# Kernel optimization log

Hardware: AMD Instinct MI355X
Metric: run time of the kernel (lower is better)

Reference implementation:

```python
import jax, jax.numpy as jnp
import numpy as np

B, T, D = 4, 2048, 2048
H = 16
DH = D // H  # 128
THETA = 10000.0


def _rope(x, offset=0):
    # x: [b, h, t, d]; lucidrains rotary_embedding_torch style (interleaved pairs)
    d = x.shape[-1]
    t = x.shape[-2]
    inv_freq = 1.0 / (THETA ** (jnp.arange(0, d, 2, dtype=jnp.float32) / d))  # [d/2]
    pos = jnp.arange(offset, offset + t, dtype=jnp.float32)
    freqs = pos[:, None] * inv_freq[None, :]              # [t, d/2]
    freqs = jnp.repeat(freqs, 2, axis=-1)                 # [t, d] (n r) interleave
    cos = jnp.cos(freqs).astype(x.dtype)
    sin = jnp.sin(freqs).astype(x.dtype)
    x1 = x[..., 0::2]
    x2 = x[..., 1::2]
    rot = jnp.stack([-x2, x1], axis=-1).reshape(x.shape)  # rotate_half
    return x * cos + rot * sin


def setup_inputs() -> dict:
    key = jax.random.key(0)
    ks = jax.random.split(key, 5)
    s = 1.0 / np.sqrt(D)
    return {
        "x": jax.random.normal(ks[0], (B, T, D), jnp.float32),
        "Wq": jax.random.normal(ks[1], (D, D), jnp.float32) * s,
        "Wk": jax.random.normal(ks[2], (D, D), jnp.float32) * s,
        "Wv": jax.random.normal(ks[3], (D, D), jnp.float32) * s,
        "Wo": jax.random.normal(ks[4], (D, D), jnp.float32) * s,
    }


def reference(x, Wq, Wk, Wv, Wo):
    b, t, d = x.shape
    # QKV projections (bias-free), split heads: b t (h f) -> b h t f
    q = (x @ Wq).reshape(b, t, H, DH).transpose(0, 2, 1, 3)
    k = (x @ Wk).reshape(b, t, H, DH).transpose(0, 2, 1, 3)
    v = (x @ Wv).reshape(b, t, H, DH).transpose(0, 2, 1, 3)
    # rotary embedding on q and k (offset = 0)
    q = _rope(q)
    k = _rope(k)
    # causal scaled dot-product attention
    scale = 1.0 / np.sqrt(DH)
    logits = jnp.einsum('bhtf,bhsf->bhts', q, k) * scale
    causal = jnp.tril(jnp.ones((t, t), dtype=bool))
    logits = jnp.where(causal, logits, jnp.finfo(logits.dtype).min)
    p = jax.nn.softmax(logits, axis=-1)
    y = jnp.einsum('bhts,bhsf->bhtf', p, v)
    # b h t f -> b t (h f), then output projection
    y = y.transpose(0, 2, 1, 3).reshape(b, t, d)
    return y @ Wo
```

## Files before the change

### kernel.cpp

```cpp
#include <hip/hip_runtime.h>
#include <hip/hip_bf16.h>
#include <math.h>

typedef unsigned short u16;
typedef __attribute__((ext_vector_type(8))) __bf16 bf16x8;
typedef __attribute__((ext_vector_type(4))) float f32x4;
typedef __attribute__((ext_vector_type(16))) float f32x16;
typedef __attribute__((ext_vector_type(8))) u16 u16x8;
typedef __attribute__((ext_vector_type(4))) u16 u16x4;
typedef __attribute__((ext_vector_type(4))) unsigned u32x4;

#define T_SEQ 2048
#define DMODEL 2048
#define NH 16
#define DHEAD 128
#define BATCH 4
#define QKV_STR 6144
#define ATTN_SCALE 0.08838834764831845f
#define QSCALE_LOG2E 0.1275411278534803f

#define GLOAD(gp, lp) __builtin_amdgcn_global_load_lds( \
    (const __attribute__((address_space(1))) void*)(gp), \
    (__attribute__((address_space(3))) void*)(lp), 16, 0, 0)

#define BAR() __builtin_amdgcn_s_barrier()
#define LGKM0() asm volatile("s_waitcnt lgkmcnt(0)" ::: "memory")
#define VMCNT4() asm volatile("s_waitcnt vmcnt(4)" ::: "memory")
#define MFMA32(A, B, C) __builtin_amdgcn_mfma_f32_32x32x16_bf16(A, B, C, 0, 0, 0)

__device__ __forceinline__ float b2f(u16 u) {
  union { float f; unsigned int i; } x; x.i = ((unsigned int)u) << 16; return x.f;
}
__device__ __forceinline__ u16 f2b(float f) {
  __bf16 h = (__bf16)f;
  return *(u16*)&h;
}
__device__ __forceinline__ unsigned pk2(float lo, float hi2) {
  __bf16 a = (__bf16)lo, b = (__bf16)hi2;
  unsigned short ua = *(unsigned short*)&a, ub = *(unsigned short*)&b;
  return (unsigned)ua | ((unsigned)ub << 16);
}

__global__ __launch_bounds__(256) void cast_f32_bf16(const float* __restrict__ in,
                                                     u16* __restrict__ out) {
  long i = ((long)blockIdx.x * 256 + threadIdx.x) * 8;
  float4 a = *(const float4*)(in + i);
  float4 b = *(const float4*)(in + i + 4);
  u16x8 r;
  r[0] = f2b(a.x); r[1] = f2b(a.y); r[2] = f2b(a.z); r[3] = f2b(a.w);
  r[4] = f2b(b.x); r[5] = f2b(b.y); r[6] = f2b(b.z); r[7] = f2b(b.w);
  *(u16x8*)(out + i) = r;
}

__global__ __launch_bounds__(256) void wtrans4_kernel(const float* __restrict__ W0,
                                                      const float* __restrict__ W1,
                                                      const float* __restrict__ W2,
                                                      const float* __restrict__ W3,
                                                      u16* __restrict__ WtBase) {
  __shared__ float tile[64][65];
  const int z = blockIdx.z;
  const float* W = (z == 0) ? W0 : (z == 1) ? W1 : (z == 2) ? W2 : W3;
  u16* Wt = WtBase + (long)z * 4194304;
  const int k0 = blockIdx.x * 64, n0 = blockIdx.y * 64;
  const int c = threadIdx.x & 63, r4 = threadIdx.x >> 6;
#pragma unroll
  for (int p = 0; p < 16; p++) {
    int r = p * 4 + r4;
    tile[r][c] = W[(long)(k0 + r) * DMODEL + n0 + c];
  }
  __syncthreads();
#pragma unroll
  for (int p = 0; p < 16; p++) {
    int r = p * 4 + r4;
    Wt[(long)(n0 + r) * DMODEL + k0 + c] = f2b(tile[c][r]);
  }
}

__global__ __launch_bounds__(256) void vtrans_kernel(const u16* __restrict__ C,
                                                     u16* __restrict__ Vt) {
  __shared__ u16 tile[64][66];
  const int s0 = blockIdx.x * 64, f0 = blockIdx.y * 64;
  const int bh = blockIdx.z;
  const int b = bh >> 4, h = bh & 15;
  const int c = threadIdx.x & 63, r4 = threadIdx.x >> 6;
#pragma unroll
  for (int p = 0; p < 16; p++) {
    int r = p * 4 + r4;
    tile[r][c] = C[(long)(b * T_SEQ + s0 + r) * QKV_STR + 4096 + h * DHEAD + f0 + c];
  }
  __syncthreads();
#pragma unroll
  for (int p = 0; p < 16; p++) {
    int r = p * 4 + r4;
    Vt[(long)(bh * DHEAD + f0 + r) * T_SEQ + s0 + c] = tile[c][r];
  }
}

__global__ __launch_bounds__(256) void rope_qk_kernel(u16* __restrict__ X) {
  int idx = blockIdx.x * 256 + threadIdx.x;
  int c8 = idx & 511;
  long row = idx >> 9;
  int t = (int)(row & (T_SEQ - 1));
  int i4 = c8 & 15;
  long off = row * QKV_STR + (long)c8 * 8;
  u16x8 v = *(u16x8*)(X + off);
  float o[8];
#pragma unroll
  for (int j = 0; j < 4; j++) {
    int i = i4 * 4 + j;
    float inv = __builtin_amdgcn_exp2f((float)i * -0.20762050593045857f);
    float ang = (float)t * inv;
    float cs = cosf(ang), sn = sinf(ang);
    float x0 = b2f(v[2 * j]), x1 = b2f(v[2 * j + 1]);
    o[2 * j]     = x0 * cs - x1 * sn;
    o[2 * j + 1] = x1 * cs + x0 * sn;
  }
  u16x8 r;
#pragma unroll
  for (int j = 0; j < 8; j++) r[j] = f2b(o[j]);
  *(u16x8*)(X + off) = r;
}

#define LOAD_A(q)                                                      \
  _Pragma("unroll") for (int k = 0; k < 2; k++)                        \
  _Pragma("unroll") for (int m = 0; m < 2; m++) {                      \
    int r = wr * 128 + (q) * 32 + m * 16 + lr;                         \
    int cc = (k * 4 + lc) ^ (r & 7);                                   \
    a[k][m] = *(const bf16x8*)&sA[par][r * 64 + cc * 8];               \
  }

#define LOAD_B()                                                       \
  _Pragma("unroll") for (int k = 0; k < 2; k++)                        \
  _Pragma("unroll") for (int n = 0; n < 4; n++) {                      \
    int r = wc * 64 + n * 16 + lr;                                     \
    int cc = (k * 4 + lc) ^ (r & 7);                                   \
    b[k][n] = *(const bf16x8*)&sB[par][r * 64 + cc * 8];               \
  }

#define MFMA_QUAD(q)                                                   \
  _Pragma("unroll") for (int k = 0; k < 2; k++)                        \
  _Pragma("unroll") for (int n = 0; n < 4; n++)                        \
  _Pragma("unroll") for (int m = 0; m < 2; m++)                        \
    acc[(q) * 2 + m][n] = __builtin_amdgcn_mfma_f32_16x16x32_bf16(     \
        a[k][m], b[k][n], acc[(q) * 2 + m][n], 0, 0, 0);

#define STAGE_HALF(g, ld, ldsp, rc0, t_, h_)                           \
  _Pragma("unroll") for (int j = 0; j < 2; j++) {                      \
    int rl = (h_) * 128 + wid * 16 + j * 8 + (lane >> 3);              \
    int cc = (lane & 7) ^ (lane >> 3);                                 \
    GLOAD((g) + ((rc0) + rl) * (long)(ld) + (long)(t_) * 64 + cc * 8,  \
          (ldsp) + (h_) * 128 * 64 + (wid * 16 + j * 8) * 64);         \
  }

template <int OUT_F32>
__global__ __launch_bounds__(512, 2) void gemm_bt(const u16* __restrict__ A, long lda,
                                                  const u16* __restrict__ Bt,
                                                  void* __restrict__ Cv,
                                                  int M, int N, int K) {
  __shared__ u16 sA[2][256 * 64];
  __shared__ u16 sB[2][256 * 64];
  const int tid = threadIdx.x, lane = tid & 63, wid = tid >> 6;
  const int wr = wid >> 2, wc = wid & 3;
  const int lr = lane & 15, lc = lane >> 4;
  const int id = blockIdx.x;
  const int per = (N >> 8) >> 3;
  const int g8 = id >> 3;
  const long col0 = (long)((id & 7) + 8 * (g8 % per)) * 256;
  const long row0 = (long)(g8 / per) * 256;
  const int NT = K >> 6;

  f32x4 acc[8][4] = {};
  bf16x8 a[2][2], b[2][4];

  STAGE_HALF(Bt, K, &sB[0][0], col0, 0, 0);
  STAGE_HALF(Bt, K, &sB[0][0], col0, 0, 1);
  STAGE_HALF(A, lda, &sA[0][0], row0, 0, 0);
  STAGE_HALF(A, lda, &sA[0][0], row0, 0, 1);
  STAGE_HALF(Bt, K, &sB[1][0], col0, 1, 0);
  STAGE_HALF(Bt, K, &sB[1][0], col0, 1, 1);
  VMCNT4();
  BAR();

#pragma unroll 2
  for (int t = 0; t < NT; t++) {
    const int par = t & 1;
    LOAD_B();
    LOAD_A(0);
    if (t + 1 < NT) { STAGE_HALF(A, lda, &sA[par ^ 1][0], row0, t + 1, 0); }
    BAR(); LGKM0();
    __builtin_amdgcn_s_setprio(1); MFMA_QUAD(0); __builtin_amdgcn_s_setprio(0);
    BAR();
    LOAD_A(1);
    if (t + 1 < NT) { STAGE_HALF(A, lda, &sA[par ^ 1][0], row0, t + 1, 1); }
    if (t + 2 < NT) { STAGE_HALF(Bt, K, &sB[par][0], col0, t + 2, 0); }
    BAR(); LGKM0();
    __builtin_amdgcn_s_setprio(1); MFMA_QUAD(1); __builtin_amdgcn_s_setprio(0);
    BAR();
    LOAD_A(2);
    if (t + 2 < NT) { STAGE_HALF(Bt, K, &sB[par][0], col0, t + 2, 1); }
    BAR(); LGKM0();
    __builtin_amdgcn_s_setprio(1); MFMA_QUAD(2); __builtin_amdgcn_s_setprio(0);
    BAR();
    LOAD_A(3);
    VMCNT4();
    BAR(); LGKM0();
    __builtin_amdgcn_s_setprio(1); MFMA_QUAD(3); __builtin_amdgcn_s_setprio(0);
    BAR();
  }

#pragma unroll
  for (int mf = 0; mf < 8; mf++)
#pragma unroll
    for (int n = 0; n < 4; n++)
#pragma unroll
      for (int i = 0; i < 4; i++) {
        long row = row0 + wr * 128 + mf * 16 + lc * 4 + i;
        long col = col0 + wc * 64 + n * 16 + lr;
        float v = acc[mf][n][i];
        if (OUT_F32) ((float*)Cv)[row * N + col] = v;
        else ((u16*)Cv)[row * N + col] = f2b(v);
      }
}

__global__ __launch_bounds__(256, 2) void attn_kernel(const u16* __restrict__ QK,
                                                      const u16* __restrict__ Vt) {
  __shared__ u16 lK[2][64 * 128];
  __shared__ u16 lV[2][128 * 64];
  const int tid = threadIdx.x, lane = tid & 63, w = tid >> 6;
  const int hi = lane >> 5, l31 = lane & 31;
  const int id = blockIdx.x;
  const int qt = 15 - (id >> 6);
  const int bh = id & 63;
  const int b = bh >> 4, h = bh & 15;
  const int qg = qt * 128 + w * 32 + l31;
  const int swz = l31 & 7;

  bf16x8 qf[8];
  const long qrow = (long)(b * T_SEQ + qg) * QKV_STR + h * DHEAD;
#pragma unroll
  for (int kd = 0; kd < 8; kd++) {
    u16x8 raw = *(const u16x8*)(QK + qrow + kd * 16 + hi * 8);
    bf16x8 q;
#pragma unroll
    for (int j = 0; j < 8; j++) q[j] = (__bf16)(b2f(raw[j]) * QSCALE_LOG2E);
    qf[kd] = q;
  }

  f32x16 o0 = {}, o1 = {}, o2 = {}, o3 = {};
  float m_st = -INFINITY, l_st = 0.f;
  const int nt = (qt + 1) * 2;

#define STAGE(nb, kt_)                                                              \
  {                                                                                 \
    _Pragma("unroll")                                                               \
    for (int j = 0; j < 4; j++) {                                                   \
      int sb = (w * 4 + j) * 64;                                                    \
      int slot = sb + lane;                                                         \
      { int r = slot >> 4, pc = slot & 15, cc = pc ^ (r & 7);                       \
        GLOAD(QK + (long)(b * T_SEQ + (kt_) * 64 + r) * QKV_STR + 2048 +            \
                  h * DHEAD + cc * 8,                                               \
              &lK[nb][sb * 8]); }                                                   \
      { int r = slot >> 3, pc = slot & 7, cc = pc ^ (r & 7);                        \
        GLOAD(Vt + (long)(bh * DHEAD + r) * T_SEQ + (kt_) * 64 + cc * 8,            \
              &lV[nb][sb * 8]); }                                                   \
    }                                                                               \
  }

  STAGE(0, 0);
  __syncthreads();

  for (int kt = 0; kt < nt; kt++) {
    const int cur = kt & 1;
    if (kt + 1 < nt) STAGE(cur ^ 1, kt + 1);

    f32x16 st0 = {}, st1 = {};
    __builtin_amdgcn_s_setprio(1);
#pragma unroll
    for (int kd = 0; kd < 8; kd++) {
      int pc = (kd * 2 + hi) ^ swz;
      bf16x8 kf0 = *(const bf16x8*)&lK[cur][l31 * 128 + pc * 8];
      bf16x8 kf1 = *(const bf16x8*)&lK[cur][(32 + l31) * 128 + pc * 8];
      st0 = MFMA32(kf0, qf[kd], st0);
      st1 = MFMA32(kf1, qf[kd], st1);
    }
    __builtin_amdgcn_s_setprio(0);

    if (kt * 64 + 63 > qt * 128 + w * 32) {
#pragma unroll
      for (int r = 0; r < 16; r++) {
        int sl = kt * 64 + (r & 3) + 8 * (r >> 2) + 4 * hi;
        if (sl > qg) st0[r] = -1e30f;
        if (sl + 32 > qg) st1[r] = -1e30f;
      }
    }

    float mx = -1e30f;
#pragma unroll
    for (int r = 0; r < 16; r++) mx = fmaxf(mx, fmaxf(st0[r], st1[r]));
    mx = fmaxf(mx, __shfl_xor(mx, 32, 64));
    if (__any(mx > m_st + 8.0f)) {
      float mnew = fmaxf(m_st, mx);
      float corr = __builtin_amdgcn_exp2f(m_st - mnew);
      m_st = mnew;
      l_st *= corr;
#pragma unroll
      for (int r = 0; r < 16; r++) {
        o0[r] *= corr; o1[r] *= corr; o2[r] *= corr; o3[r] *= corr;
      }
    }
    float rs = 0.f;
#pragma unroll
    for (int r = 0; r < 16; r++) {
      st0[r] = __builtin_amdgcn_exp2f(st0[r] - m_st); rs += st0[r];
      st1[r] = __builtin_amdgcn_exp2f(st1[r] - m_st); rs += st1[r];
    }
    l_st += rs + __shfl_xor(rs, 32, 64);

    __builtin_amdgcn_s_setprio(1);
#define PVHALF(stX, sb)                                                        \
    _Pragma("unroll")                                                          \
    for (int g = 0; g < 2; g++) {                                              \
      unsigned A0 = pk2(stX[8 * g + 0], stX[8 * g + 1]);                       \
      unsigned A1 = pk2(stX[8 * g + 2], stX[8 * g + 3]);                       \
      unsigned B0 = pk2(stX[8 * g + 4], stX[8 * g + 5]);                       \
      unsigned B1 = pk2(stX[8 * g + 6], stX[8 * g + 7]);                       \
      unsigned xA0 = __shfl_xor(A0, 32, 64);                                   \
      unsigned xA1 = __shfl_xor(A1, 32, 64);                                   \
      unsigned xB0 = __shfl_xor(B0, 32, 64);                                   \
      unsigned xB1 = __shfl_xor(B1, 32, 64);                                   \
      u32x4 pw;                                                                \
      pw[0] = hi ? xB0 : A0;                                                   \
      pw[1] = hi ? xB1 : A1;                                                   \
      pw[2] = hi ? B0 : xA0;                                                   \
      pw[3] = hi ? B1 : xA1;                                                   \
      bf16x8 pa = *(bf16x8*)&pw;                                               \
      const int ks = (sb) * 2 + g;                                             \
      int pc0 = (ks * 2 + hi) ^ swz;                                           \
      bf16x8 vb0 = *(const bf16x8*)&lV[cur][(l31) * 64 + pc0 * 8];             \
      o0 = MFMA32(vb0, pa, o0);                                                \
      bf16x8 vb1 = *(const bf16x8*)&lV[cur][(32 + l31) * 64 + pc0 * 8];        \
      o1 = MFMA32(vb1, pa, o1);                                                \
      bf16x8 vb2 = *(const bf16x8*)&lV[cur][(64 + l31) * 64 + pc0 * 8];        \
      o2 = MFMA32(vb2, pa, o2);                                                \
      bf16x8 vb3 = *(const bf16x8*)&lV[cur][(96 + l31) * 64 + pc0 * 8];        \
      o3 = MFMA32(vb3, pa, o3);                                                \
    }
    PVHALF(st0, 0)
    PVHALF(st1, 1)
#undef PVHALF
    __builtin_amdgcn_s_setprio(0);

    __syncthreads();
  }

  float inv = __builtin_amdgcn_rcpf(l_st);
#define WR(oN, n)                                                              \
  _Pragma("unroll")                                                            \
  for (int rq = 0; rq < 4; rq++) {                                             \
    u16x4 pk;                                                                  \
    _Pragma("unroll")                                                          \
    for (int j = 0; j < 4; j++) pk[j] = f2b(oN[rq * 4 + j] * inv);             \
    *(u16x4*)((u16*)QK + qrow + 4096 + (n) * 32 + rq * 8 + hi * 4) = pk;       \
  }
  WR(o0, 0) WR(o1, 1) WR(o2, 2) WR(o3, 3)
#undef WR
#undef STAGE
}

extern "C" void kernel_launch(void* const* d_in, const int* in_sizes, int n_in,
                              void* d_out, int out_size, void* d_ws, size_t ws_size,
                              hipStream_t stream) {
  const float* x  = (const float*)d_in[0];
  const float* Wq = (const float*)d_in[1];
  const float* Wk = (const float*)d_in[2];
  const float* Wv = (const float*)d_in[3];
  const float* Wo = (const float*)d_in[4];
  float* out = (float*)d_out;
  char* ws = (char*)d_ws;

  const long MB = 1048576L;
  u16* xb   = (u16*)(ws);
  u16* Wt4  = (u16*)(ws + 32 * MB);
  u16* Cqkv = (u16*)(ws + 64 * MB);
  u16* Vtb  = xb;

  cast_f32_bf16<<<8192, 256, 0, stream>>>(x, xb);
  dim3 wt_g(32, 32, 4);
  wtrans4_kernel<<<wt_g, 256, 0, stream>>>(Wq, Wk, Wv, Wo, Wt4);

  gemm_bt<0><<<768, 512, 0, stream>>>(xb, 2048, Wt4, Cqkv, 8192, 6144, 2048);

  rope_qk_kernel<<<16384, 256, 0, stream>>>(Cqkv);

  dim3 vt_g(32, 2, 64);
  vtrans_kernel<<<vt_g, 256, 0, stream>>>(Cqkv, Vtb);

  attn_kernel<<<1024, 256, 0, stream>>>(Cqkv, Vtb);

  gemm_bt<1><<<256, 512, 0, stream>>>(Cqkv + 4096, QKV_STR, Wt4 + 3 * 4194304L,
                                      (void*)out, 8192, 2048, 2048);
}
```

Measured before the change: 444.6 us.

## Fuse RoPE into QKV GEMM epilogue and drop explicit lgkmcnt waits

Applies rotary embedding to Q and K in the epilogue of the QKV projection GEMM, pairing even and odd columns through a lane shuffle. This removes the separate rope kernel, which read and wrote the Q and K halves of the buffer a second time. The explicit lgkmcnt(0) waits before each MFMA quad are also removed, leaving LDS load ordering to the compiler. The fast __sinf/__cosf intrinsics can lose accuracy at large angles (positions up to 2047), and the shuffle adds work to the epilogue.

```diff
diff --git a/kernel.cpp b/kernel.cpp
--- a/kernel.cpp
+++ b/kernel.cpp
@@ -24,7 +24,6 @@
     (__attribute__((address_space(3))) void*)(lp), 16, 0, 0)
 
 #define BAR() __builtin_amdgcn_s_barrier()
-#define LGKM0() asm volatile("s_waitcnt lgkmcnt(0)" ::: "memory")
 #define VMCNT4() asm volatile("s_waitcnt vmcnt(4)" ::: "memory")
 #define MFMA32(A, B, C) __builtin_amdgcn_mfma_f32_32x32x16_bf16(A, B, C, 0, 0, 0)
 
@@ -96,31 +95,6 @@
   }
 }
 
-__global__ __launch_bounds__(256) void rope_qk_kernel(u16* __restrict__ X) {
-  int idx = blockIdx.x * 256 + threadIdx.x;
-  int c8 = idx & 511;
-  long row = idx >> 9;
-  int t = (int)(row & (T_SEQ - 1));
-  int i4 = c8 & 15;
-  long off = row * QKV_STR + (long)c8 * 8;
-  u16x8 v = *(u16x8*)(X + off);
-  float o[8];
-#pragma unroll
-  for (int j = 0; j < 4; j++) {
-    int i = i4 * 4 + j;
-    float inv = __builtin_amdgcn_exp2f((float)i * -0.20762050593045857f);
-    float ang = (float)t * inv;
-    float cs = cosf(ang), sn = sinf(ang);
-    float x0 = b2f(v[2 * j]), x1 = b2f(v[2 * j + 1]);
-    o[2 * j]     = x0 * cs - x1 * sn;
-    o[2 * j + 1] = x1 * cs + x0 * sn;
-  }
-  u16x8 r;
-#pragma unroll
-  for (int j = 0; j < 8; j++) r[j] = f2b(o[j]);
-  *(u16x8*)(X + off) = r;
-}
-
 #define LOAD_A(q)                                                      \
   _Pragma("unroll") for (int k = 0; k < 2; k++)                        \
   _Pragma("unroll") for (int m = 0; m < 2; m++) {                      \
@@ -152,7 +126,7 @@
           (ldsp) + (h_) * 128 * 64 + (wid * 16 + j * 8) * 64);         \
   }
 
-template <int OUT_F32>
+template <int OUT_F32, int ROPE>
 __global__ __launch_bounds__(512, 2) void gemm_bt(const u16* __restrict__ A, long lda,
                                                   const u16* __restrict__ Bt,
                                                   void* __restrict__ Cv,
@@ -187,27 +161,28 @@
     LOAD_B();
     LOAD_A(0);
     if (t + 1 < NT) { STAGE_HALF(A, lda, &sA[par ^ 1][0], row0, t + 1, 0); }
-    BAR(); LGKM0();
+    BAR();
     __builtin_amdgcn_s_setprio(1); MFMA_QUAD(0); __builtin_amdgcn_s_setprio(0);
     BAR();
     LOAD_A(1);
     if (t + 1 < NT) { STAGE_HALF(A, lda, &sA[par ^ 1][0], row0, t + 1, 1); }
     if (t + 2 < NT) { STAGE_HALF(Bt, K, &sB[par][0], col0, t + 2, 0); }
-    BAR(); LGKM0();
+    BAR();
     __builtin_amdgcn_s_setprio(1); MFMA_QUAD(1); __builtin_amdgcn_s_setprio(0);
     BAR();
     LOAD_A(2);
     if (t + 2 < NT) { STAGE_HALF(Bt, K, &sB[par][0], col0, t + 2, 1); }
-    BAR(); LGKM0();
+    BAR();
     __builtin_amdgcn_s_setprio(1); MFMA_QUAD(2); __builtin_amdgcn_s_setprio(0);
     BAR();
     LOAD_A(3);
     VMCNT4();
-    BAR(); LGKM0();
+    BAR();
     __builtin_amdgcn_s_setprio(1); MFMA_QUAD(3); __builtin_amdgcn_s_setprio(0);
     BAR();
   }
 
+  const bool doRope = ROPE && (col0 < 4096);
 #pragma unroll
   for (int mf = 0; mf < 8; mf++)
 #pragma unroll
@@ -217,6 +192,15 @@
         long row = row0 + wr * 128 + mf * 16 + lc * 4 + i;
         long col = col0 + wc * 64 + n * 16 + lr;
         float v = acc[mf][n][i];
+        if (doRope) {
+          float other = __shfl_xor(v, 1, 64);
+          int tt = (int)(row & (T_SEQ - 1));
+          int pi = ((int)col & 127) >> 1;
+          float ang = (float)tt *
+                      __builtin_amdgcn_exp2f((float)pi * -0.20762050593045857f);
+          float cs = __cosf(ang), sn = __sinf(ang);
+          v = (lr & 1) ? (v * cs + other * sn) : (v * cs - other * sn);
+        }
         if (OUT_F32) ((float*)Cv)[row * N + col] = v;
         else ((u16*)Cv)[row * N + col] = f2b(v);
       }
@@ -388,15 +372,13 @@
   dim3 wt_g(32, 32, 4);
   wtrans4_kernel<<<wt_g, 256, 0, stream>>>(Wq, Wk, Wv, Wo, Wt4);
 
-  gemm_bt<0><<<768, 512, 0, stream>>>(xb, 2048, Wt4, Cqkv, 8192, 6144, 2048);
-
-  rope_qk_kernel<<<16384, 256, 0, stream>>>(Cqkv);
+  gemm_bt<0, 1><<<768, 512, 0, stream>>>(xb, 2048, Wt4, Cqkv, 8192, 6144, 2048);
 
   dim3 vt_g(32, 2, 64);
   vtrans_kernel<<<vt_g, 256, 0, stream>>>(Cqkv, Vtb);
 
   attn_kernel<<<1024, 256, 0, stream>>>(Cqkv, Vtb);
 
-  gemm_bt<1><<<256, 512, 0, stream>>>(Cqkv + 4096, QKV_STR, Wt4 + 3 * 4194304L,
-                                      (void*)out, 8192, 2048, 2048);
-}
+  gemm_bt<1, 0><<<256, 512, 0, stream>>>(Cqkv + 4096, QKV_STR, Wt4 + 3 * 4194304L,
+                                         (void*)out, 8192, 2048, 2048);
+}
```

Result: faster. 433.0 us (-2.6%).
